# Optimization experiments

Hardware: AMD Instinct MI355X
Metric: run time of the kernel (lower is better)

Reference implementation:

```python
import jax, jax.numpy as jnp
import numpy as np

N_BINS = 18
EPS = 1e-9


def setup_inputs() -> dict:
    key = jax.random.key(0)
    k1, k2 = jax.random.split(key)
    # pha: phase values in [-pi, pi], shape (B, C, Fp, S, T)
    pha = jax.random.uniform(k1, (4, 16, 10, 4, 2048), dtype=jnp.float32,
                             minval=-np.pi, maxval=np.pi)
    # amp: non-negative amplitude envelope, shape (B, C, Fa, S, T)
    amp = jax.random.uniform(k2, (4, 16, 30, 4, 2048), dtype=jnp.float32)
    return {"pha": pha, "amp": amp}


def reference(pha, amp):
    # Bin cutoffs: linspace(-pi, pi, n_bins+1), matching the torch buffer.
    cutoffs = jnp.linspace(-np.pi, np.pi, N_BINS + 1, dtype=jnp.float32)
    # torch.bucketize(right=False) == searchsorted side='left'; then -1, clamp.
    bins = jnp.clip(jnp.searchsorted(cutoffs, pha, side='left') - 1, 0, N_BINS - 1)
    # One-hot mask over phase bins: (B, C, Fp, S, T, K)
    onehot = jax.nn.one_hot(bins, N_BINS, dtype=amp.dtype)
    # Per-bin amplitude sums, contracting over time t (avoids the torch 7D tensor):
    # amp_sums[b,c,p,a,s,k] = sum_t onehot[b,c,p,s,t,k] * amp[b,c,a,s,t]
    amp_sums = jnp.einsum('bcpstk,bcast->bcpask', onehot, amp)  # (B,C,Fp,Fa,S,K)
    counts = onehot.sum(axis=4)  # (B, C, Fp, S, K)
    amp_means = amp_sums / (counts[:, :, :, None] + EPS)  # broadcast over Fa
    amp_probs = amp_means / (amp_means.sum(axis=-1, keepdims=True) + EPS)
    # Negative entropy term over bins: (B, C, Fp, Fa, S)
    ent = (amp_probs * jnp.log(amp_probs + EPS)).sum(axis=-1)
    MI = (jnp.log(N_BINS + EPS) + ent) / jnp.log(jnp.float32(N_BINS))
    # Mean over segments -> (B, C, Fp, Fa)
    return MI.mean(axis=-1)
```

## Files before the change

### kernel.cpp

```cpp
#include <hip/hip_runtime.h>
#include <math.h>


#define FP_ 10
#define FA_ 30
#define K_  18
#define T_  2048
#define TH_ 1024
#define TC_ 256
#define NTILE 4
#define NT_ 512

#define OFF_BINS 128
#define BINROW   1040
#define BSW_     260
#define OFF_LO   (OFF_BINS + FP_ * BINROW)
#define PROW     272
#define PLSZ     (32 * PROW)
#define OFF_HI   (OFF_LO + PLSZ)
#define LDS_TOTAL (OFF_HI + PLSZ)
#define OFF_RED  128
#define OFF_CNT  (OFF_RED + 192 * 33 * 4)

typedef int i32x4 __attribute__((ext_vector_type(4)));

static __device__ __forceinline__ unsigned oh8(unsigned w, unsigned kb4) {
  const unsigned x = w ^ kb4;
  const unsigned t = (x & 0x7F7F7F7Fu) + 0x7F7F7F7Fu;
  return ((~(t | x)) & 0x80808080u) >> 7;
}

__global__ __launch_bounds__(NT_, 4)
void mi_main(const float* __restrict__ pha, const float* __restrict__ amp,
             float* __restrict__ ws) {
  extern __shared__ unsigned char smem[];
  float*    c_lds = (float*)smem;
  unsigned* binsw = (unsigned*)(smem + OFF_BINS);
  float*    red   = (float*)(smem + OFF_RED);
  int*      cnt_t = (int*)(smem + OFF_CNT);

  const int tid  = threadIdx.x;
  const int lane = tid & 63;
  const int wv   = tid >> 6;
  const int quad = lane >> 4;
  const int lc   = lane & 15;
  const int mq   = wv & 3;
  const int q2   = wv >> 2;

  const int bid  = blockIdx.x;
  const int g    = bid >> 1;
  const int half = bid & 1;
  const int s    = g & 3;
  const int bc   = g >> 2;
  const long pha_base = (long)bc * (FP_ * 4L * T_) + (long)s * T_ + half * TH_;
  const long amp_base = (long)bc * (FA_ * 4L * T_) + (long)s * T_ + half * TH_;

  if (tid < 19) {
    const double PI_D = 3.14159265358979323846264338327950288;
    const double step = (2.0 * PI_D) / 18.0;
    c_lds[tid] = (tid == 18) ? (float)PI_D : (float)(-PI_D + (double)tid * step);
  }
  if (tid < 17) {
    *(uint4*)(smem + OFF_LO + 30 * PROW + tid * 16) =
        make_uint4(0x01010101u, 0x01010101u, 0x01010101u, 0x01010101u);
    *(uint4*)(smem + OFF_LO + 31 * PROW + tid * 16) = make_uint4(0u, 0u, 0u, 0u);
    *(uint4*)(smem + OFF_HI + 30 * PROW + tid * 16) = make_uint4(0u, 0u, 0u, 0u);
    *(uint4*)(smem + OFF_HI + 31 * PROW + tid * 16) = make_uint4(0u, 0u, 0u, 0u);
  }

  const bool stager = tid < 480;
  const int a_row = tid >> 4;
  const int seg   = tid & 15;
  const float* gsrc = amp + amp_base + (long)a_row * (4L * T_) + seg * 16;
  float4 vreg[4];
  if (stager) {
    #pragma unroll
    for (int j = 0; j < 4; ++j) vreg[j] = *(const float4*)(gsrc + j * 4);
  }

  const float PI_F    = 3.14159274101257324f;
  const float INVSTEP = 2.8647890f;
  #pragma unroll
  for (int it = 0; it < 5; ++it) {
    const int i = it * NT_ + tid;
    const int p = i >> 8, w = i & 255;
    const float4 v = *(const float4*)(pha + pha_base + (long)p * (4L * T_) + w * 4);
    const float xs[4] = {v.x, v.y, v.z, v.w};
    unsigned pk = 0;
    #pragma unroll
    for (int j = 0; j < 4; ++j) {
      const float x = xs[j];
      int gi = (int)((x + PI_F) * INVSTEP);
      gi = min(17, max(0, gi));
      if (x <= c_lds[gi]) gi -= 1;
      else if (x > c_lds[gi + 1]) gi += 1;
      gi = min(17, max(0, gi));
      pk |= ((unsigned)gi) << (8 * j);
    }
    binsw[p * BSW_ + w] = pk;
  }

  int p_mt[3]; unsigned kb4_mt[3];
  #pragma unroll
  for (int mt = 0; mt < 3; ++mt) {
    const int row = mq * 48 + mt * 16 + lc;
    int p = row / 18; p = min(p, 9);
    const unsigned kb = (unsigned)(row - p * 18);
    p_mt[mt] = p;
    kb4_mt[mt] = kb * 0x01010101u;
  }

  i32x4 accl[3][2], acch[3][2];
  #pragma unroll
  for (int mt = 0; mt < 3; ++mt) {
    accl[mt][0] = (i32x4){0,0,0,0}; accl[mt][1] = (i32x4){0,0,0,0};
    acch[mt][0] = (i32x4){0,0,0,0}; acch[mt][1] = (i32x4){0,0,0,0};
  }
  __syncthreads();

  #pragma unroll 1
  for (int tile = 0; tile < NTILE; ++tile) {
    if (stager) {
      unsigned lo[4], hi[4];
      #pragma unroll
      for (int j = 0; j < 4; ++j) {
        const float xv[4] = {vreg[j].x, vreg[j].y, vreg[j].z, vreg[j].w};
        unsigned q[4];
        #pragma unroll
        for (int e = 0; e < 4; ++e)
          q[e] = min((unsigned)(xv[e] * 65536.0f), 65535u);
        const unsigned w01 = q[0] | (q[1] << 16);
        const unsigned w23 = q[2] | (q[3] << 16);
        lo[j] = __builtin_amdgcn_perm(w23, w01, 0x06040200u) ^ 0x80808080u;
        hi[j] = __builtin_amdgcn_perm(w23, w01, 0x07050301u) ^ 0x80808080u;
      }
      *(uint4*)(smem + OFF_LO + a_row * PROW + seg * 16) = make_uint4(lo[0], lo[1], lo[2], lo[3]);
      *(uint4*)(smem + OFF_HI + a_row * PROW + seg * 16) = make_uint4(hi[0], hi[1], hi[2], hi[3]);
    }
    __syncthreads();
    if (stager && tile < NTILE - 1) {
      #pragma unroll
      for (int j = 0; j < 4; ++j)
        vreg[j] = *(const float4*)(gsrc + (tile + 1) * TC_ + j * 4);
    }

    #pragma unroll
    for (int ci = 0; ci < 2; ++ci) {
      const int cl = q2 * 2 + ci;
      const unsigned char* bl = smem + OFF_LO + cl * 64 + quad * 16;
      const unsigned char* bh = smem + OFF_HI + cl * 64 + quad * 16;
      const i32x4 Bl0 = *(const i32x4*)(bl + lc * PROW);
      const i32x4 Bl1 = *(const i32x4*)(bl + (16 + lc) * PROW);
      const i32x4 Bh0 = *(const i32x4*)(bh + lc * PROW);
      const i32x4 Bh1 = *(const i32x4*)(bh + (16 + lc) * PROW);
      const int chg = tile * 4 + cl;
      #pragma unroll
      for (int mt = 0; mt < 3; ++mt) {
        const uint4 wb = *(const uint4*)(smem + OFF_BINS + p_mt[mt] * BINROW
                                         + chg * 64 + quad * 16);
        const unsigned kb4 = kb4_mt[mt];
        const i32x4 A = (i32x4){(int)oh8(wb.x, kb4), (int)oh8(wb.y, kb4),
                                (int)oh8(wb.z, kb4), (int)oh8(wb.w, kb4)};
        accl[mt][0] = __builtin_amdgcn_mfma_i32_16x16x64_i8(A, Bl0, accl[mt][0], 0, 0, 0);
        acch[mt][0] = __builtin_amdgcn_mfma_i32_16x16x64_i8(A, Bh0, acch[mt][0], 0, 0, 0);
        accl[mt][1] = __builtin_amdgcn_mfma_i32_16x16x64_i8(A, Bl1, accl[mt][1], 0, 0, 0);
        acch[mt][1] = __builtin_amdgcn_mfma_i32_16x16x64_i8(A, Bh1, acch[mt][1], 0, 0, 0);
      }
    }
    __syncthreads();
  }

  if (lc == 14) {
    #pragma unroll
    for (int mt = 0; mt < 3; ++mt)
      #pragma unroll
      for (int r = 0; r < 4; ++r)
        cnt_t[q2 * 192 + mq * 48 + mt * 16 + quad * 4 + r] = accl[mt][1][r];
  }
  __syncthreads();

  float vals[3][2][4];
  #pragma unroll
  for (int mt = 0; mt < 3; ++mt)
    #pragma unroll
    for (int n = 0; n < 2; ++n)
      #pragma unroll
      for (int r = 0; r < 4; ++r) {
        const int row = mq * 48 + mt * 16 + quad * 4 + r;
        const int cnt = cnt_t[q2 * 192 + row];
        const int raw = (acch[mt][n][r] << 8) + accl[mt][n][r] + 32896 * cnt;
        float v = (float)raw * 1.52587890625e-5f;
        if (n == 1 && lc == 14) v = (float)accl[mt][n][r];
        vals[mt][n][r] = v;
      }
  __syncthreads();

  if (q2 == 1) {
    float* S = &red[mq * 48 * 33];
    #pragma unroll
    for (int mt = 0; mt < 3; ++mt)
      #pragma unroll
      for (int n = 0; n < 2; ++n)
        #pragma unroll
        for (int r = 0; r < 4; ++r)
          S[(mt * 16 + quad * 4 + r) * 33 + n * 16 + lc] = vals[mt][n][r];
  }
  __syncthreads();
  if (q2 == 0) {
    float* S = &red[mq * 48 * 33];
    float* W = ws + (long)bid * 6144;
    #pragma unroll
    for (int mt = 0; mt < 3; ++mt)
      #pragma unroll
      for (int n = 0; n < 2; ++n)
        #pragma unroll
        for (int r = 0; r < 4; ++r) {
          const float v = vals[mt][n][r] + S[(mt * 16 + quad * 4 + r) * 33 + n * 16 + lc];
          W[(mq * 48 + mt * 16 + quad * 4 + r) * 32 + n * 16 + lc] = v;
        }
  }
}

__global__ __launch_bounds__(256)
void mi_ent(const float* __restrict__ ws, float* __restrict__ out) {
  __shared__ float tbl[8 * 576];
  __shared__ float red[4][32];
  const int bc = blockIdx.x / FP_;
  const int p  = blockIdx.x - bc * FP_;
  const int tid = threadIdx.x;

  #pragma unroll
  for (int it = 0; it < 18; ++it) {
    const int i = it * 256 + tid;
    const int sub = i / 576, r = i - sub * 576;
    tbl[i] = ws[(long)(bc * 8 + sub) * 6144 + p * 576 + r];
  }
  __syncthreads();

  if (tid < 120) {
    const int s = tid / FA_;
    const int a = tid - s * FA_;
    const float* t0 = &tbl[(2 * s) * 576];
    const float* t1 = &tbl[(2 * s + 1) * 576];
    float m[K_];
    float tot = 0.0f;
    #pragma unroll
    for (int k = 0; k < K_; ++k) {
      const float cnt = t0[k * 32 + 30] + t1[k * 32 + 30];
      const float sv  = t0[k * 32 + a]  + t1[k * 32 + a];
      const float mk  = sv / (cnt + 1e-9f);
      m[k] = mk;
      tot += mk;
    }
    const float denom = tot + 1e-9f;
    float ent = 0.0f;
    #pragma unroll
    for (int k = 0; k < K_; ++k) {
      const float pr = m[k] / denom;
      ent += pr * logf(pr + 1e-9f);
    }
    const float L = logf(18.0f);
    red[s][a] = (L + ent) / L;
  }
  __syncthreads();
  if (tid < FA_)
    out[(bc * FP_ + p) * FA_ + tid] =
        0.25f * (red[0][tid] + red[1][tid] + red[2][tid] + red[3][tid]);
}

extern "C" void kernel_launch(void* const* d_in, const int* in_sizes, int n_in,
                              void* d_out, int out_size, void* d_ws, size_t ws_size,
                              hipStream_t stream) {
  const float* pha = (const float*)d_in[0];
  const float* amp = (const float*)d_in[1];
  float* out = (float*)d_out;
  float* ws  = (float*)d_ws;

  hipLaunchKernelGGL(mi_main, dim3(512), dim3(NT_), LDS_TOTAL, stream, pha, amp, ws);
  hipLaunchKernelGGL(mi_ent, dim3(64 * FP_), dim3(256), 0, stream, ws, out);
}
```

Before: 112.2 us.

## Fuse entropy stage into main kernel with full-time-per-block and atomic output

Each block now processes the full time axis of one (b,c,s) segment instead of half, doubling NTILE and the LDS bin buffer, and halving the grid to 256 blocks. The partial-sum workspace and the separate entropy kernel are removed: the block reduces its counts and sums in LDS, computes MI for all (p,a) pairs itself, and atomically adds the per-segment contribution into a zeroed output. This removes a second launch and the workspace round trip, at the cost of fewer blocks than CUs, lower occupancy (launch bounds 2), a memset, and atomic float adds.

```diff
diff --git a/kernel.cpp b/kernel.cpp
--- a/kernel.cpp
+++ b/kernel.cpp
@@ -6,21 +6,20 @@
 #define FA_ 30
 #define K_  18
 #define T_  2048
-#define TH_ 1024
 #define TC_ 256
-#define NTILE 4
+#define NTILE 8
 #define NT_ 512
 
 #define OFF_BINS 128
-#define BINROW   1040
-#define BSW_     260
+#define BINROW   2064
+#define BSW_     516
 #define OFF_LO   (OFF_BINS + FP_ * BINROW)
 #define PROW     272
 #define PLSZ     (32 * PROW)
 #define OFF_HI   (OFF_LO + PLSZ)
 #define LDS_TOTAL (OFF_HI + PLSZ)
 #define OFF_RED  128
-#define OFF_CNT  (OFF_RED + 192 * 33 * 4)
+#define OFF_CNT  25472
 
 typedef int i32x4 __attribute__((ext_vector_type(4)));
 
@@ -30,9 +29,9 @@
   return ((~(t | x)) & 0x80808080u) >> 7;
 }
 
-__global__ __launch_bounds__(NT_, 4)
+__global__ __launch_bounds__(NT_, 2)
 void mi_main(const float* __restrict__ pha, const float* __restrict__ amp,
-             float* __restrict__ ws) {
+             float* __restrict__ out) {
   extern __shared__ unsigned char smem[];
   float*    c_lds = (float*)smem;
   unsigned* binsw = (unsigned*)(smem + OFF_BINS);
@@ -47,13 +46,11 @@
   const int mq   = wv & 3;
   const int q2   = wv >> 2;
 
-  const int bid  = blockIdx.x;
-  const int g    = bid >> 1;
-  const int half = bid & 1;
-  const int s    = g & 3;
-  const int bc   = g >> 2;
-  const long pha_base = (long)bc * (FP_ * 4L * T_) + (long)s * T_ + half * TH_;
-  const long amp_base = (long)bc * (FA_ * 4L * T_) + (long)s * T_ + half * TH_;
+  const int g  = blockIdx.x;
+  const int s  = g & 3;
+  const int bc = g >> 2;
+  const long pha_base = (long)bc * (FP_ * 4L * T_) + (long)s * T_;
+  const long amp_base = (long)bc * (FA_ * 4L * T_) + (long)s * T_;
 
   if (tid < 19) {
     const double PI_D = 3.14159265358979323846264338327950288;
@@ -80,11 +77,9 @@
 
   const float PI_F    = 3.14159274101257324f;
   const float INVSTEP = 2.8647890f;
-  #pragma unroll
-  for (int it = 0; it < 5; ++it) {
-    const int i = it * NT_ + tid;
-    const int p = i >> 8, w = i & 255;
-    const float4 v = *(const float4*)(pha + pha_base + (long)p * (4L * T_) + w * 4);
+  #pragma unroll 2
+  for (int p = 0; p < FP_; ++p) {
+    const float4 v = *(const float4*)(pha + pha_base + (long)p * (4L * T_) + tid * 4);
     const float xs[4] = {v.x, v.y, v.z, v.w};
     unsigned pk = 0;
     #pragma unroll
@@ -97,7 +92,7 @@
       gi = min(17, max(0, gi));
       pk |= ((unsigned)gi) << (8 * j);
     }
-    binsw[p * BSW_ + w] = pk;
+    binsw[p * BSW_ + tid] = pk;
   }
 
   int p_mt[3]; unsigned kb4_mt[3];
@@ -208,46 +203,27 @@
   __syncthreads();
   if (q2 == 0) {
     float* S = &red[mq * 48 * 33];
-    float* W = ws + (long)bid * 6144;
     #pragma unroll
     for (int mt = 0; mt < 3; ++mt)
       #pragma unroll
       for (int n = 0; n < 2; ++n)
         #pragma unroll
         for (int r = 0; r < 4; ++r) {
-          const float v = vals[mt][n][r] + S[(mt * 16 + quad * 4 + r) * 33 + n * 16 + lc];
-          W[(mq * 48 + mt * 16 + quad * 4 + r) * 32 + n * 16 + lc] = v;
+          const int idx = (mt * 16 + quad * 4 + r) * 33 + n * 16 + lc;
+          S[idx] = vals[mt][n][r] + S[idx];
         }
   }
-}
-
-__global__ __launch_bounds__(256)
-void mi_ent(const float* __restrict__ ws, float* __restrict__ out) {
-  __shared__ float tbl[8 * 576];
-  __shared__ float red[4][32];
-  const int bc = blockIdx.x / FP_;
-  const int p  = blockIdx.x - bc * FP_;
-  const int tid = threadIdx.x;
-
-  #pragma unroll
-  for (int it = 0; it < 18; ++it) {
-    const int i = it * 256 + tid;
-    const int sub = i / 576, r = i - sub * 576;
-    tbl[i] = ws[(long)(bc * 8 + sub) * 6144 + p * 576 + r];
-  }
-  __syncthreads();
-
-  if (tid < 120) {
-    const int s = tid / FA_;
-    const int a = tid - s * FA_;
-    const float* t0 = &tbl[(2 * s) * 576];
-    const float* t1 = &tbl[(2 * s + 1) * 576];
+  __syncthreads();
+
+  if (tid < FP_ * FA_) {
+    const int p = tid / FA_;
+    const int a = tid - p * FA_;
     float m[K_];
     float tot = 0.0f;
     #pragma unroll
     for (int k = 0; k < K_; ++k) {
-      const float cnt = t0[k * 32 + 30] + t1[k * 32 + 30];
-      const float sv  = t0[k * 32 + a]  + t1[k * 32 + a];
+      const float cnt = red[(p * K_ + k) * 33 + 30];
+      const float sv  = red[(p * K_ + k) * 33 + a];
       const float mk  = sv / (cnt + 1e-9f);
       m[k] = mk;
       tot += mk;
@@ -259,13 +235,10 @@
       const float pr = m[k] / denom;
       ent += pr * logf(pr + 1e-9f);
     }
-    const float L = logf(18.0f);
-    red[s][a] = (L + ent) / L;
-  }
-  __syncthreads();
-  if (tid < FA_)
-    out[(bc * FP_ + p) * FA_ + tid] =
-        0.25f * (red[0][tid] + red[1][tid] + red[2][tid] + red[3][tid]);
+    const float L  = logf(18.0f);
+    const float mi = (L + ent) / L;
+    atomicAdd(&out[(bc * FP_ + p) * FA_ + a], 0.25f * mi);
+  }
 }
 
 extern "C" void kernel_launch(void* const* d_in, const int* in_sizes, int n_in,
@@ -274,8 +247,7 @@
   const float* pha = (const float*)d_in[0];
   const float* amp = (const float*)d_in[1];
   float* out = (float*)d_out;
-  float* ws  = (float*)d_ws;
-
-  hipLaunchKernelGGL(mi_main, dim3(512), dim3(NT_), LDS_TOTAL, stream, pha, amp, ws);
-  hipLaunchKernelGGL(mi_ent, dim3(64 * FP_), dim3(256), 0, stream, ws, out);
+
+  hipMemsetAsync(d_out, 0, (size_t)out_size * sizeof(float), stream);
+  hipLaunchKernelGGL(mi_main, dim3(256), dim3(NT_), LDS_TOTAL, stream, pha, amp, out);
 }
```

Result: slower. 116.0 us (+3.4%).
